# Kernel optimization log

Measured on AMD Instinct MI355X. Metric: run time of the kernel, lower is better.

Reference implementation:

```python
import jax, jax.numpy as jnp
import numpy as np

DROPOUT_P = 0.2
HEAD_SIZE = 64
EMBED = 1024


def setup_inputs() -> dict:
    key = jax.random.key(0)
    kx, kk, kq, kv = jax.random.split(key, 4)
    B, T = 4, 4096
    x = jax.random.normal(kx, (B, T, EMBED), dtype=jnp.float32)
    # torch Linear(embed, head, bias=False): y = x @ W.T with W [head, embed].
    # We store W_* as [embed, head] so projection is x @ W.
    scale = 1.0 / np.sqrt(EMBED)
    Wk = jax.random.uniform(kk, (EMBED, HEAD_SIZE), jnp.float32, -scale, scale)
    Wq = jax.random.uniform(kq, (EMBED, HEAD_SIZE), jnp.float32, -scale, scale)
    Wv = jax.random.uniform(kv, (EMBED, HEAD_SIZE), jnp.float32, -scale, scale)
    return {"x": x, "Wk": Wk, "Wq": Wq, "Wv": Wv}


def reference(x, Wk, Wq, Wv):
    # Projections: [B,T,E] @ [E,H] -> [B,T,H]
    k = jnp.einsum("bte,eh->bth", x, Wk)
    q = jnp.einsum("bte,eh->bth", x, Wq)
    v = jnp.einsum("bte,eh->bth", x, Wv)
    # Raw scaled scores, NO softmax: [B,T,T]
    w = jnp.einsum("bqh,bkh->bqk", q, k) * (HEAD_SIZE ** -0.5)
    # Dropout (training mode, inverted scaling) with a fixed key.
    keep = jax.random.bernoulli(jax.random.key(42), 1.0 - DROPOUT_P, w.shape)
    w = jnp.where(keep, w / (1.0 - DROPOUT_P), 0.0)
    # Weighted V sum: [B,T,T] @ [B,T,H] -> [B,T,H]
    return jnp.einsum("bqk,bkh->bqh", w, v)
```

## Files before the change

### kernel.cpp

```cpp
#include <hip/hip_runtime.h>


#define TB 4
#define TT 4096
#define TE 1024
#define TH 64
#define COMB_SCALE 0.15625f

typedef __bf16 bf16x8 __attribute__((ext_vector_type(8)));
typedef __bf16 bf16x4 __attribute__((ext_vector_type(4)));
typedef float  f32x4  __attribute__((ext_vector_type(4)));

__device__ __forceinline__ unsigned rotl32(unsigned x, int d) {
  return (x << d) | (x >> (32 - d));
}

__device__ __forceinline__ unsigned tf_bits(unsigned j) {
  const unsigned ks1 = 42u;
  const unsigned ks2 = 0x1BD11BDAu ^ 42u;
  unsigned x0 = 0u, x1 = j + ks1;
#define TF_RND(d) { x0 += x1; x1 = rotl32(x1, (d)); x1 ^= x0; }
  TF_RND(13) TF_RND(15) TF_RND(26) TF_RND(6)
  x0 += ks1; x1 += ks2 + 1u;
  TF_RND(17) TF_RND(29) TF_RND(16) TF_RND(24)
  x0 += ks2; x1 += 0u + 2u;
  TF_RND(13) TF_RND(15) TF_RND(26) TF_RND(6)
  x0 += 0u;  x1 += ks1 + 3u;
  TF_RND(17) TF_RND(29) TF_RND(16) TF_RND(24)
  x0 += ks1; x1 += ks2 + 4u;
  TF_RND(13) TF_RND(15) TF_RND(26) TF_RND(6)
  x0 += ks2; x1 += 0u + 5u;
#undef TF_RND
  return x0 ^ x1;
}

__device__ __forceinline__ bool tf_keep(unsigned j) {
  return (tf_bits(j) >> 9) < 6710887u;
}

__global__ __launch_bounds__(256)
void prep_wt(const float* __restrict__ Wq, const float* __restrict__ Wk,
             const float* __restrict__ Wv, __bf16* __restrict__ WT)
{
  __shared__ float lds[64][65];
  const int wi = blockIdx.x >> 4;
  const int k0 = (blockIdx.x & 15) * 64;
  const float* W = (wi == 0) ? Wq : ((wi == 1) ? Wk : Wv);
  const int tid = threadIdx.x;
#pragma unroll
  for (int it = 0; it < 16; ++it) {
    const int idx = tid + it * 256;
    lds[idx >> 6][idx & 63] = W[(size_t)(k0 + (idx >> 6)) * TH + (idx & 63)];
  }
  __syncthreads();
#pragma unroll
  for (int it = 0; it < 16; ++it) {
    const int idx = tid + it * 256;
    const int n = idx >> 6, kk = idx & 63;
    WT[(size_t)(wi * TH + n) * TE + k0 + kk] = (__bf16)lds[kk][n];
  }
}

__global__ __launch_bounds__(256)
void proj_mfma(const float* __restrict__ x, const __bf16* __restrict__ WT,
               __bf16* __restrict__ qs, __bf16* __restrict__ ks,
               __bf16* __restrict__ vT)
{
  const int tid = threadIdx.x;
  const int w  = tid >> 6, l = tid & 63;
  const int l4 = l >> 4,  lm = l & 15;
  const int rh = w >> 1,  ch = w & 1;
  const int R  = blockIdx.x * 32 + rh * 16;

  const float*  xr = x  + (size_t)(R + lm) * TE;
  const __bf16* wt = WT + (size_t)(ch * 96 + lm) * TE;

  f32x4 acc[6];
#pragma unroll
  for (int t = 0; t < 6; ++t) acc[t] = (f32x4){0.f, 0.f, 0.f, 0.f};

  for (int k0 = 0; k0 < TE; k0 += 32) {
    const float4 u0 = *reinterpret_cast<const float4*>(xr + k0 + l4 * 8);
    const float4 u1 = *reinterpret_cast<const float4*>(xr + k0 + l4 * 8 + 4);
    bf16x8 am;
    am[0] = (__bf16)u0.x; am[1] = (__bf16)u0.y;
    am[2] = (__bf16)u0.z; am[3] = (__bf16)u0.w;
    am[4] = (__bf16)u1.x; am[5] = (__bf16)u1.y;
    am[6] = (__bf16)u1.z; am[7] = (__bf16)u1.w;
    bf16x8 bn[6];
#pragma unroll
    for (int t = 0; t < 6; ++t)
      bn[t] = *reinterpret_cast<const bf16x8*>(wt + (size_t)t * 16 * TE + k0 + l4 * 8);
#pragma unroll
    for (int t = 0; t < 6; ++t)
      acc[t] = __builtin_amdgcn_mfma_f32_16x16x32_bf16(am, bn[t], acc[t], 0, 0, 0);
  }

  const int row0 = R + l4 * 4;
#pragma unroll
  for (int t = 0; t < 6; ++t) {
    const int n = ch * 96 + t * 16 + lm;
    if (n < TH) {
#pragma unroll
      for (int r = 0; r < 4; ++r)
        qs[(size_t)(row0 + r) * TH + n] = (__bf16)(acc[t][r] * COMB_SCALE);
    } else if (n < 2 * TH) {
#pragma unroll
      for (int r = 0; r < 4; ++r)
        ks[(size_t)(row0 + r) * TH + (n - TH)] = (__bf16)acc[t][r];
    } else {
      bf16x4 vv;
#pragma unroll
      for (int r = 0; r < 4; ++r) vv[r] = (__bf16)acc[t][r];
      const int bb = row0 >> 12, trow = row0 & (TT - 1);
      *reinterpret_cast<bf16x4*>(
          vT + ((size_t)(bb * TH + (n - 2 * TH)) * TT + trow)) = vv;
    }
  }
}

__global__ __launch_bounds__(256)
void attn_mfma(const __bf16* __restrict__ qs,
               const __bf16* __restrict__ ks,
               const __bf16* __restrict__ vT,
               float* __restrict__ out)
{
  __shared__ __bf16 S_lds[4][16 * 64];
  __shared__ float  Oex[3][16][TH + 1];

  const int tid = threadIdx.x;
  const int w   = tid >> 6;
  const int l   = tid & 63;
  const int l4  = l >> 4;
  const int lm  = l & 15;

  const int b     = blockIdx.x >> 8;
  const int qt16  = blockIdx.x & 255;
  const int qrow0 = qt16 * 16;
  const int kv0   = w * (TT / 4);

  const __bf16* qb = qs + ((size_t)b * TT + qrow0) * TH;
  const bf16x8 qf0 = *reinterpret_cast<const bf16x8*>(qb + (size_t)lm * TH + l4 * 8);
  const bf16x8 qf1 = *reinterpret_cast<const bf16x8*>(qb + (size_t)lm * TH + 32 + l4 * 8);

  const __bf16* kbp = ks + (size_t)b * TT * TH;
  const __bf16* vbp = vT + (size_t)b * TH * TT;

  f32x4 o_acc[4];
#pragma unroll
  for (int t = 0; t < 4; ++t) o_acc[t] = (f32x4){0.f, 0.f, 0.f, 0.f};

  const unsigned base0 = ((unsigned)(b * TT) + (unsigned)qrow0 + (unsigned)(l4 * 4)) * (unsigned)TT;
  const unsigned sw = (unsigned)((lm & 7) << 3);

  for (int kb = kv0; kb < kv0 + TT / 4; kb += 64) {
    bf16x8 kf[4][2];
#pragma unroll
    for (int t = 0; t < 4; ++t) {
      const __bf16* kr = kbp + (size_t)(kb + t * 16 + lm) * TH;
#pragma unroll
      for (int s = 0; s < 2; ++s)
        kf[t][s] = *reinterpret_cast<const bf16x8*>(kr + s * 32 + l4 * 8);
    }

    f32x4 sa[4];
#pragma unroll
    for (int t = 0; t < 4; ++t) {
      f32x4 c = {0.f, 0.f, 0.f, 0.f};
      c = __builtin_amdgcn_mfma_f32_16x16x32_bf16(qf0, kf[t][0], c, 0, 0, 0);
      c = __builtin_amdgcn_mfma_f32_16x16x32_bf16(qf1, kf[t][1], c, 0, 0, 0);
      sa[t] = c;
    }

    bf16x8 vf[4][2];
#pragma unroll
    for (int t = 0; t < 4; ++t) {
      const __bf16* vr = vbp + (size_t)(t * 16 + lm) * TT + kb;
#pragma unroll
      for (int s = 0; s < 2; ++s)
        vf[t][s] = *reinterpret_cast<const bf16x8*>(vr + s * 32 + l4 * 8);
    }

    const unsigned jcol = (unsigned)kb + (unsigned)lm;
#pragma unroll
    for (int t = 0; t < 4; ++t) {
#pragma unroll
      for (int r = 0; r < 4; ++r) {
        const unsigned j = base0 + (unsigned)(r * TT) + jcol + (unsigned)(t * 16);
        const float svv = tf_keep(j) ? sa[t][r] : 0.0f;
        const int row = l4 * 4 + r;
        const int col = t * 16 + lm;
        S_lds[w][row * 64 + (col ^ ((row & 7) << 3))] = (__bf16)svv;
      }
    }

    const bf16x8 af0 = *reinterpret_cast<const bf16x8*>(
        &S_lds[w][lm * 64 + ((unsigned)(l4 * 8) ^ sw)]);
    const bf16x8 af1 = *reinterpret_cast<const bf16x8*>(
        &S_lds[w][lm * 64 + ((unsigned)(32 + l4 * 8) ^ sw)]);

#pragma unroll
    for (int t = 0; t < 4; ++t) {
      o_acc[t] = __builtin_amdgcn_mfma_f32_16x16x32_bf16(af0, vf[t][0], o_acc[t], 0, 0, 0);
      o_acc[t] = __builtin_amdgcn_mfma_f32_16x16x32_bf16(af1, vf[t][1], o_acc[t], 0, 0, 0);
    }
  }

  if (w > 0) {
#pragma unroll
    for (int t = 0; t < 4; ++t)
#pragma unroll
      for (int r = 0; r < 4; ++r)
        Oex[w - 1][l4 * 4 + r][t * 16 + lm] = o_acc[t][r];
  }
  __syncthreads();
  if (w == 0) {
    float* outb = out + ((size_t)b * TT + qrow0) * TH;
#pragma unroll
    for (int t = 0; t < 4; ++t)
#pragma unroll
      for (int r = 0; r < 4; ++r) {
        const int row = l4 * 4 + r, col = t * 16 + lm;
        const float v = o_acc[t][r] + Oex[0][row][col] + Oex[1][row][col] +
                        Oex[2][row][col];
        outb[(size_t)row * TH + col] = v;
      }
  }
}

extern "C" void kernel_launch(void* const* d_in, const int* in_sizes, int n_in,
                              void* d_out, int out_size, void* d_ws, size_t ws_size,
                              hipStream_t stream) {
  const float* x  = (const float*)d_in[0];
  const float* Wk = (const float*)d_in[1];
  const float* Wq = (const float*)d_in[2];
  const float* Wv = (const float*)d_in[3];
  float* outp = (float*)d_out;

  const size_t SZ = (size_t)TB * TT * TH;
  __bf16* q_ws  = (__bf16*)d_ws;
  __bf16* k_ws  = q_ws + SZ;
  __bf16* vT_ws = k_ws + SZ;
  __bf16* WT_ws = vT_ws + SZ;

  prep_wt<<<dim3(48), dim3(256), 0, stream>>>(Wq, Wk, Wv, WT_ws);
  proj_mfma<<<dim3(TB * TT / 32), dim3(256), 0, stream>>>(
      x, WT_ws, q_ws, k_ws, vT_ws);
  attn_mfma<<<dim3(TB * (TT / 16)), dim3(256), 0, stream>>>(
      q_ws, k_ws, vT_ws, outp);
}
```

Baseline: 221.5 us.

## Split attention KV range across 8 waves with tree reduction and cheaper RNG ops

The attention kernel now runs 512 threads per block, so 8 waves each cover an eighth of the key range. Partial outputs are combined in LDS with a three-step tree reduction that adds extra barriers. Separately, the Threefry rotate uses the alignbit intrinsic and the keep test compares the raw 32-bit value against a threshold, dropping a shift. The aim is more waves in flight to hide memory latency and fewer ALU ops in the dropout hash, which is the dominant compute, at the cost of extra synchronization and launch-bounds register pressure.

```diff
diff --git a/kernel.cpp b/kernel.cpp
--- a/kernel.cpp
+++ b/kernel.cpp
@@ -11,31 +11,29 @@
 typedef __bf16 bf16x4 __attribute__((ext_vector_type(4)));
 typedef float  f32x4  __attribute__((ext_vector_type(4)));
 
-__device__ __forceinline__ unsigned rotl32(unsigned x, int d) {
-  return (x << d) | (x >> (32 - d));
-}
+#define ROTL(x, d) __builtin_amdgcn_alignbit((x), (x), 32u - (d))
 
 __device__ __forceinline__ unsigned tf_bits(unsigned j) {
   const unsigned ks1 = 42u;
   const unsigned ks2 = 0x1BD11BDAu ^ 42u;
   unsigned x0 = 0u, x1 = j + ks1;
-#define TF_RND(d) { x0 += x1; x1 = rotl32(x1, (d)); x1 ^= x0; }
-  TF_RND(13) TF_RND(15) TF_RND(26) TF_RND(6)
+#define TF_RND(d) { x0 += x1; x1 = ROTL(x1, (d)); x1 ^= x0; }
+  TF_RND(13u) TF_RND(15u) TF_RND(26u) TF_RND(6u)
   x0 += ks1; x1 += ks2 + 1u;
-  TF_RND(17) TF_RND(29) TF_RND(16) TF_RND(24)
+  TF_RND(17u) TF_RND(29u) TF_RND(16u) TF_RND(24u)
   x0 += ks2; x1 += 0u + 2u;
-  TF_RND(13) TF_RND(15) TF_RND(26) TF_RND(6)
+  TF_RND(13u) TF_RND(15u) TF_RND(26u) TF_RND(6u)
   x0 += 0u;  x1 += ks1 + 3u;
-  TF_RND(17) TF_RND(29) TF_RND(16) TF_RND(24)
+  TF_RND(17u) TF_RND(29u) TF_RND(16u) TF_RND(24u)
   x0 += ks1; x1 += ks2 + 4u;
-  TF_RND(13) TF_RND(15) TF_RND(26) TF_RND(6)
+  TF_RND(13u) TF_RND(15u) TF_RND(26u) TF_RND(6u)
   x0 += ks2; x1 += 0u + 5u;
 #undef TF_RND
   return x0 ^ x1;
 }
 
 __device__ __forceinline__ bool tf_keep(unsigned j) {
-  return (tf_bits(j) >> 9) < 6710887u;
+  return tf_bits(j) < 3435974144u;
 }
 
 __global__ __launch_bounds__(256)
@@ -119,14 +117,14 @@
   }
 }
 
-__global__ __launch_bounds__(256)
+__global__ __launch_bounds__(512, 8)
 void attn_mfma(const __bf16* __restrict__ qs,
                const __bf16* __restrict__ ks,
                const __bf16* __restrict__ vT,
                float* __restrict__ out)
 {
-  __shared__ __bf16 S_lds[4][16 * 64];
-  __shared__ float  Oex[3][16][TH + 1];
+  __shared__ __bf16 S_lds[8][16 * 64];
+  __shared__ float  Oex[4][16][TH + 4];
 
   const int tid = threadIdx.x;
   const int w   = tid >> 6;
@@ -137,7 +135,7 @@
   const int b     = blockIdx.x >> 8;
   const int qt16  = blockIdx.x & 255;
   const int qrow0 = qt16 * 16;
-  const int kv0   = w * (TT / 4);
+  const int kv0   = w * (TT / 8);
 
   const __bf16* qb = qs + ((size_t)b * TT + qrow0) * TH;
   const bf16x8 qf0 = *reinterpret_cast<const bf16x8*>(qb + (size_t)lm * TH + l4 * 8);
@@ -153,7 +151,7 @@
   const unsigned base0 = ((unsigned)(b * TT) + (unsigned)qrow0 + (unsigned)(l4 * 4)) * (unsigned)TT;
   const unsigned sw = (unsigned)((lm & 7) << 3);
 
-  for (int kb = kv0; kb < kv0 + TT / 4; kb += 64) {
+  for (int kb = kv0; kb < kv0 + TT / 8; kb += 64) {
     bf16x8 kf[4][2];
 #pragma unroll
     for (int t = 0; t < 4; ++t) {
@@ -206,12 +204,44 @@
     }
   }
 
-  if (w > 0) {
-#pragma unroll
-    for (int t = 0; t < 4; ++t)
-#pragma unroll
-      for (int r = 0; r < 4; ++r)
-        Oex[w - 1][l4 * 4 + r][t * 16 + lm] = o_acc[t][r];
+  if (w >= 4) {
+#pragma unroll
+    for (int t = 0; t < 4; ++t)
+#pragma unroll
+      for (int r = 0; r < 4; ++r)
+        Oex[w - 4][l4 * 4 + r][t * 16 + lm] = o_acc[t][r];
+  }
+  __syncthreads();
+  if (w < 4) {
+#pragma unroll
+    for (int t = 0; t < 4; ++t)
+#pragma unroll
+      for (int r = 0; r < 4; ++r)
+        o_acc[t][r] += Oex[w][l4 * 4 + r][t * 16 + lm];
+  }
+  __syncthreads();
+  if (w == 2 || w == 3) {
+#pragma unroll
+    for (int t = 0; t < 4; ++t)
+#pragma unroll
+      for (int r = 0; r < 4; ++r)
+        Oex[w - 2][l4 * 4 + r][t * 16 + lm] = o_acc[t][r];
+  }
+  __syncthreads();
+  if (w < 2) {
+#pragma unroll
+    for (int t = 0; t < 4; ++t)
+#pragma unroll
+      for (int r = 0; r < 4; ++r)
+        o_acc[t][r] += Oex[w][l4 * 4 + r][t * 16 + lm];
+  }
+  __syncthreads();
+  if (w == 1) {
+#pragma unroll
+    for (int t = 0; t < 4; ++t)
+#pragma unroll
+      for (int r = 0; r < 4; ++r)
+        Oex[0][l4 * 4 + r][t * 16 + lm] = o_acc[t][r];
   }
   __syncthreads();
   if (w == 0) {
@@ -221,9 +251,7 @@
 #pragma unroll
       for (int r = 0; r < 4; ++r) {
         const int row = l4 * 4 + r, col = t * 16 + lm;
-        const float v = o_acc[t][r] + Oex[0][row][col] + Oex[1][row][col] +
-                        Oex[2][row][col];
-        outb[(size_t)row * TH + col] = v;
+        outb[(size_t)row * TH + col] = o_acc[t][r] + Oex[0][row][col];
       }
   }
 }
@@ -246,6 +274,6 @@
   prep_wt<<<dim3(48), dim3(256), 0, stream>>>(Wq, Wk, Wv, WT_ws);
   proj_mfma<<<dim3(TB * TT / 32), dim3(256), 0, stream>>>(
       x, WT_ws, q_ws, k_ws, vT_ws);
-  attn_mfma<<<dim3(TB * (TT / 16)), dim3(256), 0, stream>>>(
+  attn_mfma<<<dim3(TB * (TT / 16)), dim3(512), 0, stream>>>(
       q_ws, k_ws, vT_ws, outp);
 }
```

Result: no change. 219.7 us (-0.8%).
